# Optimization experiments

Measured on AMD Instinct MI355X. Metric: run time of the kernel, lower is better.

Reference implementation:

```python
import jax, jax.numpy as jnp
import numpy as np

B, N, C = 8, 1024, 768
H = 12
HD = C // H  # 64
SCALE = HD ** -0.5


def setup_inputs() -> dict:
    key = jax.random.key(0)
    k1, k2, k3, k4 = jax.random.split(key, 4)
    x = jax.random.normal(k1, (B, N, C), dtype=jnp.float32)
    # torch Linear weights are [out, in]; qkv has no bias (qkv_bias=False)
    w_qkv = jax.random.normal(k2, (3 * C, C), dtype=jnp.float32) * (C ** -0.5)
    w_proj = jax.random.normal(k3, (C, C), dtype=jnp.float32) * (C ** -0.5)
    b_proj = jax.random.normal(k4, (C,), dtype=jnp.float32) * 0.01
    return {"x": x, "w_qkv": w_qkv, "w_proj": w_proj, "b_proj": b_proj}


def reference(x, w_qkv, w_proj, b_proj):
    b, n, c = x.shape
    # qkv: [B, N, 3C] -> [3, B, H, N, HD]
    qkv = (x @ w_qkv.T).reshape(b, n, 3, H, c // H).transpose(2, 0, 3, 1, 4)
    q, k, v = qkv[0], qkv[1], qkv[2]
    attn = jnp.einsum('bhqd,bhkd->bhqk', q, k) * SCALE
    attn = jax.nn.softmax(attn, axis=-1)
    out = jnp.einsum('bhqk,bhkd->bhqd', attn, v)          # [B, H, N, HD]
    out = out.transpose(0, 2, 1, 3).reshape(b, n, c)      # [B, N, C]
    out = out @ w_proj.T + b_proj
    return out
```

## Files before the change

### kernel.cpp

```cpp
#include <hip/hip_runtime.h>
#include <hip/hip_bf16.h>
#include <cstdint>

#define TB 8
#define TN 1024
#define TC 768
#define TH 12
#define THD 64
#define TM (TB*TN)
#define TNQKV (3*TC)
#define QSCALE_LOG2E 0.18033688011112042f
#define THR_BITS 11.541560327111708f

typedef __attribute__((ext_vector_type(8))) short s16x8;
typedef __attribute__((ext_vector_type(4))) short s16x4;
typedef __attribute__((ext_vector_type(4))) float f32x4;
typedef __attribute__((ext_vector_type(16))) float f32x16;
typedef __attribute__((ext_vector_type(2))) unsigned int u32x2;

__device__ __forceinline__ unsigned short f2bf(float f) {
    union { float f; unsigned int u; } v; v.f = f;
    unsigned int u = v.u;
    return (unsigned short)((u + 0x7FFFu + ((u >> 16) & 1u)) >> 16);
}

__device__ __forceinline__ float bf2f(unsigned short h) {
    union { float f; unsigned int u; } v; v.u = ((unsigned int)h) << 16;
    return v.f;
}

__device__ __forceinline__ unsigned int cvt_pk_bf16(float lo, float hi) {
    unsigned int r;
    asm("v_cvt_pk_bf16_f32 %0, %1, %2" : "=v"(r) : "v"(lo), "v"(hi));
    return r;
}

__device__ __forceinline__ void gload_lds16(const unsigned short* g, unsigned short* l) {
    __builtin_amdgcn_global_load_lds(
        (const __attribute__((address_space(1))) unsigned int*)g,
        (__attribute__((address_space(3))) unsigned int*)l,
        16, 0, 0);
}

__global__ __launch_bounds__(256) void cvt3_kernel(
    const float* __restrict__ a, unsigned short* __restrict__ oa, int na,
    const float* __restrict__ b, unsigned short* __restrict__ ob, int nb,
    const float* __restrict__ c, unsigned short* __restrict__ oc, int nc)
{
    int i = blockIdx.x * blockDim.x + threadIdx.x;
    const float* src; unsigned short* dst; int idx;
    if (i < na)           { src = a; dst = oa; idx = i; }
    else if (i < na + nb) { src = b; dst = ob; idx = i - na; }
    else if (i < na + nb + nc) { src = c; dst = oc; idx = i - na - nb; }
    else return;
    f32x4 x0 = *(const f32x4*)(src + (size_t)idx * 8);
    f32x4 x1 = *(const f32x4*)(src + (size_t)idx * 8 + 4);
    s16x8 r;
    #pragma unroll
    for (int e = 0; e < 4; e++) r[e] = (short)f2bf(x0[e]);
    #pragma unroll
    for (int e = 0; e < 4; e++) r[4 + e] = (short)f2bf(x1[e]);
    *(s16x8*)(dst + (size_t)idx * 8) = r;
}

template<bool BIAS, bool OBF16, bool VSPLIT>
__global__ __launch_bounds__(256) void gemm_bt(
    const unsigned short* __restrict__ A,
    const unsigned short* __restrict__ Bm,
    void* __restrict__ Cout,
    const float* __restrict__ bias,
    unsigned short* __restrict__ vt,
    int M, int Nn, int K)
{
    __shared__ unsigned short As[128 * 64];
    __shared__ unsigned short Bs[128 * 64];
    const int t = threadIdx.x;
    const int w = t >> 6, l = t & 63;
    const int lh = l >> 4;
    const int wm = w >> 1, wn = w & 1;
    const int bm = blockIdx.x, bn = blockIdx.y;
    const int l31 = l & 31, khi = l >> 5;
    const int r7 = l31 & 7;

    f32x16 acc00 = {}, acc01 = {}, acc10 = {}, acc11 = {};

    const unsigned short* Ab = A + (size_t)bm * 128 * K;
    const unsigned short* Bb = Bm + (size_t)bn * 128 * K;

    for (int kt = 0; kt < K; kt += 64) {
        __syncthreads();
        #pragma unroll
        for (int j = 0; j < 4; j++) {
            const int s = j * 256 + t, row = s >> 3, c = s & 7;
            const int g = c ^ (row & 7);
            gload_lds16(Ab + (size_t)row * K + kt + g * 8, As + s * 8);
            gload_lds16(Bb + (size_t)row * K + kt + g * 8, Bs + s * 8);
        }
        __syncthreads();
        #pragma unroll
        for (int ks = 0; ks < 4; ks++) {
            const int ch = ((ks << 1) + khi) ^ r7;
            const unsigned short* Ar = As + (wm * 64 + l31) * 64 + ch * 8;
            const unsigned short* Br = Bs + (wn * 64 + l31) * 64 + ch * 8;
            s16x8 a0 = *(const s16x8*)(Ar);
            s16x8 a1 = *(const s16x8*)(Ar + 32 * 64);
            s16x8 b0 = *(const s16x8*)(Br);
            s16x8 b1 = *(const s16x8*)(Br + 32 * 64);
            acc00 = __builtin_amdgcn_mfma_f32_32x32x16_bf16(a0, b0, acc00, 0, 0, 0);
            acc01 = __builtin_amdgcn_mfma_f32_32x32x16_bf16(a0, b1, acc01, 0, 0, 0);
            acc10 = __builtin_amdgcn_mfma_f32_32x32x16_bf16(a1, b0, acc10, 0, 0, 0);
            acc11 = __builtin_amdgcn_mfma_f32_32x32x16_bf16(a1, b1, acc11, 0, 0, 0);
        }
    }

    const int r0 = bm * 128 + wm * 64;
    const int c0 = bn * 128 + wn * 64;
    f32x16 accs[2][2] = {{acc00, acc01}, {acc10, acc11}};
    if constexpr (VSPLIT) {
        if (bn >= 12) {
            const int bb = (r0 >> 10) * TH;
            #pragma unroll
            for (int X = 0; X < 2; X++)
                #pragma unroll
                for (int Y = 0; Y < 2; Y++) {
                    const int dg = c0 + Y * 32 + l31 - 2 * TC;
                    unsigned short* vp = vt + ((size_t)(bb + (dg >> 6)) << 16)
                                            + (dg & 63) * TN;
                    const int k0 = (r0 & 1023) + X * 32 + 4 * khi;
                    #pragma unroll
                    for (int g = 0; g < 4; g++) {
                        u32x2 r;
                        r[0] = cvt_pk_bf16(accs[X][Y][g * 4], accs[X][Y][g * 4 + 1]);
                        r[1] = cvt_pk_bf16(accs[X][Y][g * 4 + 2], accs[X][Y][g * 4 + 3]);
                        *(u32x2*)(vp + k0 + 8 * g) = r;
                    }
                }
            return;
        }
    }
    if constexpr (OBF16) {
        unsigned short* O = (unsigned short*)Cout;
        #pragma unroll
        for (int X = 0; X < 2; X++)
            #pragma unroll
            for (int Y = 0; Y < 2; Y++) {
                const int cc = c0 + Y * 32 + l31;
                const int rb = r0 + X * 32 + 4 * khi;
                #pragma unroll
                for (int i = 0; i < 16; i++)
                    O[(size_t)(rb + (i & 3) + 8 * (i >> 2)) * Nn + cc] =
                        f2bf(accs[X][Y][i]);
            }
    } else {
        float* O = (float*)Cout;
        #pragma unroll
        for (int X = 0; X < 2; X++)
            #pragma unroll
            for (int Y = 0; Y < 2; Y++) {
                const int cc = c0 + Y * 32 + l31;
                const int rb = r0 + X * 32 + 4 * khi;
                float bv = 0.f;
                if constexpr (BIAS) bv = bias[cc];
                #pragma unroll
                for (int i = 0; i < 16; i++)
                    O[(size_t)(rb + (i & 3) + 8 * (i >> 2)) * Nn + cc] =
                        accs[X][Y][i] + bv;
            }
    }
}

__global__ __launch_bounds__(512) void attn_kernel(
    const unsigned short* __restrict__ qkv,
    const unsigned short* __restrict__ vt,
    unsigned short* __restrict__ out)
{
    const int bid = blockIdx.x;
    const int vid = (bid & 7) * 96 + (bid >> 3);
    const int bh = vid >> 3;
    const int qt = vid & 7;
    const int b = bh / TH, h = bh % TH;
    const int t = threadIdx.x, w = t >> 6, l = t & 63;
    const int lr = l & 15, lh = l >> 4;
    const int qbase = qt * 128 + w * 16;

    __shared__ unsigned short Kbuf[2][64 * 64];
    __shared__ unsigned short Vbuf[2][64 * 64];
    __shared__ unsigned short plds[8][16 * 64];

    const unsigned short* kbase = qkv + (size_t)(b * TN) * TNQKV + TC + h * THD;
    const unsigned short* vtb = vt + (size_t)bh * THD * TN;

    const int srow_lo = (l >> 3);
    const int schunk = (l & 7) ^ srow_lo;
    const int srow = w * 8 + srow_lo;
    const int sdst = w * 512 + l * 8;

    const unsigned short* qptr = qkv + (size_t)(b * TN + qbase + lr) * TNQKV + h * THD;
    s16x8 bq[2];
    #pragma unroll
    for (int cj = 0; cj < 2; cj++) {
        s16x8 raw = *(const s16x8*)(qptr + cj * 32 + lh * 8);
        #pragma unroll
        for (int e = 0; e < 8; e++)
            bq[cj][e] = (short)f2bf(bf2f((unsigned short)raw[e]) * QSCALE_LOG2E);
    }
    s16x8 av1;
    #pragma unroll
    for (int e = 0; e < 8; e++) av1[e] = (short)0x3F80;

    f32x4 o[5] = {};
    float m2 = -1e30f;
    unsigned short* pw = plds[w];
    const int lr7 = lr & 7;

    gload_lds16(kbase + (size_t)srow * TNQKV + schunk * 8, &Kbuf[0][sdst]);
    gload_lds16(vtb + (size_t)srow * TN + schunk * 8, &Vbuf[0][sdst]);
    __syncthreads();

    for (int it = 0; it < 16; it++) {
        const int kt = it * 64;
        const int cur = it & 1, nxt = cur ^ 1;
        {
            const int ktn = (kt + 64) & (TN - 1);
            gload_lds16(kbase + (size_t)(ktn + srow) * TNQKV + schunk * 8, &Kbuf[nxt][sdst]);
            gload_lds16(vtb + (size_t)srow * TN + ktn + schunk * 8, &Vbuf[nxt][sdst]);
        }
        const unsigned short* Kc = Kbuf[cur];
        const unsigned short* Vc = Vbuf[cur];

        f32x4 s[4];
        #pragma unroll
        for (int kk = 0; kk < 4; kk++) {
            const int r = kk * 16 + lr;
            s16x8 ak0 = *(const s16x8*)(Kc + r * 64 + ((lh ^ lr7) * 8));
            s16x8 ak1 = *(const s16x8*)(Kc + r * 64 + (((4 + lh) ^ lr7) * 8));
            f32x4 z = {0.f, 0.f, 0.f, 0.f};
            z = __builtin_amdgcn_mfma_f32_16x16x32_bf16(ak0, bq[0], z, 0, 0, 0);
            z = __builtin_amdgcn_mfma_f32_16x16x32_bf16(ak1, bq[1], z, 0, 0, 0);
            s[kk] = z;
        }

        float v[16];
        #pragma unroll
        for (int kk = 0; kk < 4; kk++)
            #pragma unroll
            for (int i = 0; i < 4; i++) v[kk * 4 + i] = s[kk][i];
        float mx = fmaxf(fmaxf(v[0], v[1]), v[2]);
        #pragma unroll
        for (int j = 3; j + 1 < 16; j += 2) mx = fmaxf(fmaxf(mx, v[j]), v[j + 1]);
        mx = fmaxf(mx, v[15]);
        if (!__all(mx <= m2 + THR_BITS)) {
            float rmx = fmaxf(mx, __shfl_xor(mx, 16, 64));
            rmx = fmaxf(rmx, __shfl_xor(rmx, 32, 64));
            float newm = fmaxf(m2, rmx);
            float corr = __builtin_amdgcn_exp2f(m2 - newm);
            m2 = newm;
            #pragma unroll
            for (int nd = 0; nd < 5; nd++)
                #pragma unroll
                for (int i = 0; i < 4; i++) o[nd][i] *= corr;
        }
        #pragma unroll
        for (int kk = 0; kk < 4; kk++)
            #pragma unroll
            for (int i = 0; i < 4; i++)
                s[kk][i] = __builtin_amdgcn_exp2f(s[kk][i] - m2);

        #pragma unroll
        for (int kk = 0; kk < 4; kk++) {
            u32x2 pk;
            pk[0] = cvt_pk_bf16(s[kk][0], s[kk][1]);
            pk[1] = cvt_pk_bf16(s[kk][2], s[kk][3]);
            const int wch = ((kk << 1) + (lh >> 1)) ^ lr7;
            *(u32x2*)(pw + lr * 64 + wch * 8 + (lh & 1) * 4) = pk;
        }
        #pragma unroll
        for (int ktile = 0; ktile < 2; ktile++) {
            const int rch = ((ktile << 2) + lh) ^ lr7;
            s16x8 bp = *(const s16x8*)(pw + lr * 64 + rch * 8);
            #pragma unroll
            for (int nd = 0; nd < 4; nd++) {
                const int d = nd * 16 + lr;
                s16x8 av = *(const s16x8*)(
                    Vc + d * 64 + ((((ktile << 2) + lh) ^ lr7) * 8));
                o[nd] = __builtin_amdgcn_mfma_f32_16x16x32_bf16(av, bp, o[nd], 0, 0, 0);
            }
            o[4] = __builtin_amdgcn_mfma_f32_16x16x32_bf16(av1, bp, o[4], 0, 0, 0);
        }
        __syncthreads();
    }

    float inv = 1.f / o[4][0];
    unsigned short* op = out + (size_t)(b * TN + qbase + lr) * TC + h * THD;
    #pragma unroll
    for (int nd = 0; nd < 4; nd++) {
        u32x2 r;
        r[0] = cvt_pk_bf16(o[nd][0] * inv, o[nd][1] * inv);
        r[1] = cvt_pk_bf16(o[nd][2] * inv, o[nd][3] * inv);
        *(u32x2*)(op + nd * 16 + lh * 4) = r;
    }
}

extern "C" void kernel_launch(void* const* d_in, const int* in_sizes, int n_in,
                              void* d_out, int out_size, void* d_ws, size_t ws_size,
                              hipStream_t stream) {
    const float* x      = (const float*)d_in[0];
    const float* w_qkv  = (const float*)d_in[1];
    const float* w_proj = (const float*)d_in[2];
    const float* b_proj = (const float*)d_in[3];
    float* out = (float*)d_out;

    unsigned short* xb   = (unsigned short*)d_ws;
    unsigned short* wqb  = xb   + (size_t)TM * TC;
    unsigned short* wpb  = wqb  + (size_t)TNQKV * TC;
    unsigned short* qkvb = wpb  + (size_t)TC * TC;
    unsigned short* vtb  = qkvb + (size_t)TM * TNQKV;
    unsigned short* aob  = vtb  + (size_t)TB * TH * THD * TN;

    const int na = TM * TC / 8, nb = TNQKV * TC / 8, nc = TC * TC / 8;
    cvt3_kernel<<<(na + nb + nc + 255) / 256, 256, 0, stream>>>(
        x, xb, na, w_qkv, wqb, nb, w_proj, wpb, nc);

    gemm_bt<false, true, true><<<dim3(TM / 128, TNQKV / 128), 256, 0, stream>>>(
        xb, wqb, (void*)qkvb, nullptr, vtb, TM, TNQKV, TC);

    attn_kernel<<<768, 512, 0, stream>>>(qkvb, vtb, aob);

    gemm_bt<true, false, false><<<dim3(TM / 128, TC / 128), 256, 0, stream>>>(
        aob, wpb, (void*)out, b_proj, nullptr, TM, TC, TC);
}
```

Measured before the change: 113.4 us.

## Double-buffer GEMM LDS tiles with 8 waves and prioritize MFMA in attention

The GEMM kernel now uses 512 threads (8 waves, each computing a 32x64 sub-tile) and double-buffers the A/B LDS tiles, so global-to-LDS loads for the next K step overlap the MFMAs of the current one. This removes one barrier per iteration. The attention kernel stops prefetching a wrapped-around tile on its last iteration, and wraps its MFMA sections in s_setprio raises to favour matrix-core issue. In exchange the GEMM doubles its LDS use to 64KB per block, which may lower occupancy, and each wave gets less register-level reuse.

```diff
diff --git a/kernel.cpp b/kernel.cpp
--- a/kernel.cpp
+++ b/kernel.cpp
@@ -13,7 +13,6 @@
 #define THR_BITS 11.541560327111708f
 
 typedef __attribute__((ext_vector_type(8))) short s16x8;
-typedef __attribute__((ext_vector_type(4))) short s16x4;
 typedef __attribute__((ext_vector_type(4))) float f32x4;
 typedef __attribute__((ext_vector_type(16))) float f32x16;
 typedef __attribute__((ext_vector_type(2))) unsigned int u32x2;
@@ -64,7 +63,7 @@
 }
 
 template<bool BIAS, bool OBF16, bool VSPLIT>
-__global__ __launch_bounds__(256) void gemm_bt(
+__global__ __launch_bounds__(512) void gemm_bt(
     const unsigned short* __restrict__ A,
     const unsigned short* __restrict__ Bm,
     void* __restrict__ Cout,
@@ -72,100 +71,99 @@
     unsigned short* __restrict__ vt,
     int M, int Nn, int K)
 {
-    __shared__ unsigned short As[128 * 64];
-    __shared__ unsigned short Bs[128 * 64];
+    __shared__ unsigned short As[2][128 * 64];
+    __shared__ unsigned short Bs[2][128 * 64];
     const int t = threadIdx.x;
     const int w = t >> 6, l = t & 63;
-    const int lh = l >> 4;
-    const int wm = w >> 1, wn = w & 1;
+    const int wm = w & 3, wn = w >> 2;
     const int bm = blockIdx.x, bn = blockIdx.y;
     const int l31 = l & 31, khi = l >> 5;
     const int r7 = l31 & 7;
 
-    f32x16 acc00 = {}, acc01 = {}, acc10 = {}, acc11 = {};
+    f32x16 acc0 = {}, acc1 = {};
 
     const unsigned short* Ab = A + (size_t)bm * 128 * K;
     const unsigned short* Bb = Bm + (size_t)bn * 128 * K;
 
-    for (int kt = 0; kt < K; kt += 64) {
-        __syncthreads();
-        #pragma unroll
-        for (int j = 0; j < 4; j++) {
-            const int s = j * 256 + t, row = s >> 3, c = s & 7;
+    auto stage = [&](int bufi, int kt) {
+        #pragma unroll
+        for (int j = 0; j < 2; j++) {
+            const int s = j * 512 + t, row = s >> 3, c = s & 7;
             const int g = c ^ (row & 7);
-            gload_lds16(Ab + (size_t)row * K + kt + g * 8, As + s * 8);
-            gload_lds16(Bb + (size_t)row * K + kt + g * 8, Bs + s * 8);
-        }
-        __syncthreads();
+            gload_lds16(Ab + (size_t)row * K + kt + g * 8, &As[bufi][s * 8]);
+            gload_lds16(Bb + (size_t)row * K + kt + g * 8, &Bs[bufi][s * 8]);
+        }
+    };
+
+    stage(0, 0);
+    __syncthreads();
+
+    const int nkt = K / 64;
+    for (int it = 0; it < nkt; it++) {
+        const int cur = it & 1, nxt = cur ^ 1;
+        if (it + 1 < nkt) stage(nxt, (it + 1) * 64);
+        const unsigned short* Ac = As[cur];
+        const unsigned short* Bc = Bs[cur];
         #pragma unroll
         for (int ks = 0; ks < 4; ks++) {
             const int ch = ((ks << 1) + khi) ^ r7;
-            const unsigned short* Ar = As + (wm * 64 + l31) * 64 + ch * 8;
-            const unsigned short* Br = Bs + (wn * 64 + l31) * 64 + ch * 8;
-            s16x8 a0 = *(const s16x8*)(Ar);
-            s16x8 a1 = *(const s16x8*)(Ar + 32 * 64);
+            s16x8 a0 = *(const s16x8*)(Ac + (wm * 32 + l31) * 64 + ch * 8);
+            const unsigned short* Br = Bc + (wn * 64 + l31) * 64 + ch * 8;
             s16x8 b0 = *(const s16x8*)(Br);
             s16x8 b1 = *(const s16x8*)(Br + 32 * 64);
-            acc00 = __builtin_amdgcn_mfma_f32_32x32x16_bf16(a0, b0, acc00, 0, 0, 0);
-            acc01 = __builtin_amdgcn_mfma_f32_32x32x16_bf16(a0, b1, acc01, 0, 0, 0);
-            acc10 = __builtin_amdgcn_mfma_f32_32x32x16_bf16(a1, b0, acc10, 0, 0, 0);
-            acc11 = __builtin_amdgcn_mfma_f32_32x32x16_bf16(a1, b1, acc11, 0, 0, 0);
-        }
-    }
-
-    const int r0 = bm * 128 + wm * 64;
+            acc0 = __builtin_amdgcn_mfma_f32_32x32x16_bf16(a0, b0, acc0, 0, 0, 0);
+            acc1 = __builtin_amdgcn_mfma_f32_32x32x16_bf16(a0, b1, acc1, 0, 0, 0);
+        }
+        __syncthreads();
+    }
+
+    const int r0 = bm * 128 + wm * 32;
     const int c0 = bn * 128 + wn * 64;
-    f32x16 accs[2][2] = {{acc00, acc01}, {acc10, acc11}};
+    f32x16 accs[2] = {acc0, acc1};
     if constexpr (VSPLIT) {
         if (bn >= 12) {
             const int bb = (r0 >> 10) * TH;
-            #pragma unroll
-            for (int X = 0; X < 2; X++)
+            const int k0 = (r0 & 1023) + 4 * khi;
+            #pragma unroll
+            for (int Y = 0; Y < 2; Y++) {
+                const int dg = c0 + Y * 32 + l31 - 2 * TC;
+                unsigned short* vp = vt + ((size_t)(bb + (dg >> 6)) << 16)
+                                        + (dg & 63) * TN;
                 #pragma unroll
-                for (int Y = 0; Y < 2; Y++) {
-                    const int dg = c0 + Y * 32 + l31 - 2 * TC;
-                    unsigned short* vp = vt + ((size_t)(bb + (dg >> 6)) << 16)
-                                            + (dg & 63) * TN;
-                    const int k0 = (r0 & 1023) + X * 32 + 4 * khi;
-                    #pragma unroll
-                    for (int g = 0; g < 4; g++) {
-                        u32x2 r;
-                        r[0] = cvt_pk_bf16(accs[X][Y][g * 4], accs[X][Y][g * 4 + 1]);
-                        r[1] = cvt_pk_bf16(accs[X][Y][g * 4 + 2], accs[X][Y][g * 4 + 3]);
-                        *(u32x2*)(vp + k0 + 8 * g) = r;
-                    }
+                for (int g = 0; g < 4; g++) {
+                    u32x2 r;
+                    r[0] = cvt_pk_bf16(accs[Y][g * 4], accs[Y][g * 4 + 1]);
+                    r[1] = cvt_pk_bf16(accs[Y][g * 4 + 2], accs[Y][g * 4 + 3]);
+                    *(u32x2*)(vp + k0 + 8 * g) = r;
                 }
+            }
             return;
         }
     }
     if constexpr (OBF16) {
         unsigned short* O = (unsigned short*)Cout;
         #pragma unroll
-        for (int X = 0; X < 2; X++)
-            #pragma unroll
-            for (int Y = 0; Y < 2; Y++) {
-                const int cc = c0 + Y * 32 + l31;
-                const int rb = r0 + X * 32 + 4 * khi;
-                #pragma unroll
-                for (int i = 0; i < 16; i++)
-                    O[(size_t)(rb + (i & 3) + 8 * (i >> 2)) * Nn + cc] =
-                        f2bf(accs[X][Y][i]);
-            }
+        for (int Y = 0; Y < 2; Y++) {
+            const int cc = c0 + Y * 32 + l31;
+            const int rb = r0 + 4 * khi;
+            #pragma unroll
+            for (int i = 0; i < 16; i++)
+                O[(size_t)(rb + (i & 3) + 8 * (i >> 2)) * Nn + cc] =
+                    f2bf(accs[Y][i]);
+        }
     } else {
         float* O = (float*)Cout;
         #pragma unroll
-        for (int X = 0; X < 2; X++)
-            #pragma unroll
-            for (int Y = 0; Y < 2; Y++) {
-                const int cc = c0 + Y * 32 + l31;
-                const int rb = r0 + X * 32 + 4 * khi;
-                float bv = 0.f;
-                if constexpr (BIAS) bv = bias[cc];
-                #pragma unroll
-                for (int i = 0; i < 16; i++)
-                    O[(size_t)(rb + (i & 3) + 8 * (i >> 2)) * Nn + cc] =
-                        accs[X][Y][i] + bv;
-            }
+        for (int Y = 0; Y < 2; Y++) {
+            const int cc = c0 + Y * 32 + l31;
+            const int rb = r0 + 4 * khi;
+            float bv = 0.f;
+            if constexpr (BIAS) bv = bias[cc];
+            #pragma unroll
+            for (int i = 0; i < 16; i++)
+                O[(size_t)(rb + (i & 3) + 8 * (i >> 2)) * Nn + cc] =
+                    accs[Y][i] + bv;
+        }
     }
 }
 
@@ -220,8 +218,8 @@
     for (int it = 0; it < 16; it++) {
         const int kt = it * 64;
         const int cur = it & 1, nxt = cur ^ 1;
-        {
-            const int ktn = (kt + 64) & (TN - 1);
+        if (it + 1 < 16) {
+            const int ktn = kt + 64;
             gload_lds16(kbase + (size_t)(ktn + srow) * TNQKV + schunk * 8, &Kbuf[nxt][sdst]);
             gload_lds16(vtb + (size_t)srow * TN + ktn + schunk * 8, &Vbuf[nxt][sdst]);
         }
@@ -229,6 +227,7 @@
         const unsigned short* Vc = Vbuf[cur];
 
         f32x4 s[4];
+        __builtin_amdgcn_s_setprio(1);
         #pragma unroll
         for (int kk = 0; kk < 4; kk++) {
             const int r = kk * 16 + lr;
@@ -239,6 +238,7 @@
             z = __builtin_amdgcn_mfma_f32_16x16x32_bf16(ak1, bq[1], z, 0, 0, 0);
             s[kk] = z;
         }
+        __builtin_amdgcn_s_setprio(0);
 
         float v[16];
         #pragma unroll
@@ -274,6 +274,7 @@
             const int wch = ((kk << 1) + (lh >> 1)) ^ lr7;
             *(u32x2*)(pw + lr * 64 + wch * 8 + (lh & 1) * 4) = pk;
         }
+        __builtin_amdgcn_s_setprio(1);
         #pragma unroll
         for (int ktile = 0; ktile < 2; ktile++) {
             const int rch = ((ktile << 2) + lh) ^ lr7;
@@ -287,6 +288,7 @@
             }
             o[4] = __builtin_amdgcn_mfma_f32_16x16x32_bf16(av1, bp, o[4], 0, 0, 0);
         }
+        __builtin_amdgcn_s_setprio(0);
         __syncthreads();
     }
 
@@ -321,11 +323,11 @@
     cvt3_kernel<<<(na + nb + nc + 255) / 256, 256, 0, stream>>>(
         x, xb, na, w_qkv, wqb, nb, w_proj, wpb, nc);
 
-    gemm_bt<false, true, true><<<dim3(TM / 128, TNQKV / 128), 256, 0, stream>>>(
+    gemm_bt<false, true, true><<<dim3(TM / 128, TNQKV / 128), 512, 0, stream>>>(
         xb, wqb, (void*)qkvb, nullptr, vtb, TM, TNQKV, TC);
 
     attn_kernel<<<768, 512, 0, stream>>>(qkvb, vtb, aob);
 
-    gemm_bt<true, false, false><<<dim3(TM / 128, TC / 128), 256, 0, stream>>>(
+    gemm_bt<true, false, false><<<dim3(TM / 128, TC / 128), 512, 0, stream>>>(
         aob, wpb, (void*)out, b_proj, nullptr, TM, TC, TC);
 }
```

Measured after the change: 115.1 us. Within noise of the previous version (+1.5%).

## Enlarge GEMM M-tile to 256, add MFMA priority hints and skip wasted prefetch

Applied to the files above, without the earlier changes.

The GEMM kernel now computes a 256x128 tile per block, with each wave holding a 4x2 grid of 32x32 accumulators. This raises data reuse from LDS and halves the grid size for both projections. The cost is more registers and LDS per block, and fewer blocks, which can hurt occupancy and load balance (the proj GEMM drops to 192 blocks). The attention kernel also wraps its MFMA sections in s_setprio hints and skips the useless prefetch on the last iteration.

```diff
diff --git a/kernel.cpp b/kernel.cpp
--- a/kernel.cpp
+++ b/kernel.cpp
@@ -13,7 +13,6 @@
 #define THR_BITS 11.541560327111708f
 
 typedef __attribute__((ext_vector_type(8))) short s16x8;
-typedef __attribute__((ext_vector_type(4))) short s16x4;
 typedef __attribute__((ext_vector_type(4))) float f32x4;
 typedef __attribute__((ext_vector_type(16))) float f32x16;
 typedef __attribute__((ext_vector_type(2))) unsigned int u32x2;
@@ -72,76 +71,84 @@
     unsigned short* __restrict__ vt,
     int M, int Nn, int K)
 {
-    __shared__ unsigned short As[128 * 64];
+    __shared__ unsigned short As[256 * 64];
     __shared__ unsigned short Bs[128 * 64];
     const int t = threadIdx.x;
     const int w = t >> 6, l = t & 63;
-    const int lh = l >> 4;
     const int wm = w >> 1, wn = w & 1;
     const int bm = blockIdx.x, bn = blockIdx.y;
     const int l31 = l & 31, khi = l >> 5;
     const int r7 = l31 & 7;
 
-    f32x16 acc00 = {}, acc01 = {}, acc10 = {}, acc11 = {};
-
-    const unsigned short* Ab = A + (size_t)bm * 128 * K;
+    f32x16 acc[4][2] = {};
+
+    const unsigned short* Ab = A + (size_t)bm * 256 * K;
     const unsigned short* Bb = Bm + (size_t)bn * 128 * K;
 
     for (int kt = 0; kt < K; kt += 64) {
         __syncthreads();
+        #pragma unroll
+        for (int j = 0; j < 8; j++) {
+            const int s = j * 256 + t, row = s >> 3, c = s & 7;
+            const int g = c ^ (row & 7);
+            gload_lds16(Ab + (size_t)row * K + kt + g * 8, As + s * 8);
+        }
         #pragma unroll
         for (int j = 0; j < 4; j++) {
             const int s = j * 256 + t, row = s >> 3, c = s & 7;
             const int g = c ^ (row & 7);
-            gload_lds16(Ab + (size_t)row * K + kt + g * 8, As + s * 8);
             gload_lds16(Bb + (size_t)row * K + kt + g * 8, Bs + s * 8);
         }
         __syncthreads();
         #pragma unroll
         for (int ks = 0; ks < 4; ks++) {
             const int ch = ((ks << 1) + khi) ^ r7;
-            const unsigned short* Ar = As + (wm * 64 + l31) * 64 + ch * 8;
-            const unsigned short* Br = Bs + (wn * 64 + l31) * 64 + ch * 8;
-            s16x8 a0 = *(const s16x8*)(Ar);
-            s16x8 a1 = *(const s16x8*)(Ar + 32 * 64);
-            s16x8 b0 = *(const s16x8*)(Br);
-            s16x8 b1 = *(const s16x8*)(Br + 32 * 64);
-            acc00 = __builtin_amdgcn_mfma_f32_32x32x16_bf16(a0, b0, acc00, 0, 0, 0);
-            acc01 = __builtin_amdgcn_mfma_f32_32x32x16_bf16(a0, b1, acc01, 0, 0, 0);
-            acc10 = __builtin_amdgcn_mfma_f32_32x32x16_bf16(a1, b0, acc10, 0, 0, 0);
-            acc11 = __builtin_amdgcn_mfma_f32_32x32x16_bf16(a1, b1, acc11, 0, 0, 0);
-        }
-    }
-
-    const int r0 = bm * 128 + wm * 64;
+            s16x8 af[4], bf[2];
+            #pragma unroll
+            for (int X = 0; X < 4; X++)
+                af[X] = *(const s16x8*)(As + (wm * 128 + X * 32 + l31) * 64 + ch * 8);
+            #pragma unroll
+            for (int Y = 0; Y < 2; Y++)
+                bf[Y] = *(const s16x8*)(Bs + (wn * 64 + Y * 32 + l31) * 64 + ch * 8);
+            #pragma unroll
+            for (int X = 0; X < 4; X++)
+                #pragma unroll
+                for (int Y = 0; Y < 2; Y++)
+                    acc[X][Y] = __builtin_amdgcn_mfma_f32_32x32x16_bf16(
+                        af[X], bf[Y], acc[X][Y], 0, 0, 0);
+        }
+    }
+
+    const int r0 = bm * 256 + wm * 128;
     const int c0 = bn * 128 + wn * 64;
-    f32x16 accs[2][2] = {{acc00, acc01}, {acc10, acc11}};
     if constexpr (VSPLIT) {
         if (bn >= 12) {
-            const int bb = (r0 >> 10) * TH;
-            #pragma unroll
-            for (int X = 0; X < 2; X++)
+            #pragma unroll
+            for (int X = 0; X < 4; X++) {
+                const int rx = r0 + X * 32;
+                const int bb = (rx >> 10) * TH;
+                const int k0 = (rx & 1023) + 4 * khi;
                 #pragma unroll
                 for (int Y = 0; Y < 2; Y++) {
                     const int dg = c0 + Y * 32 + l31 - 2 * TC;
                     unsigned short* vp = vt + ((size_t)(bb + (dg >> 6)) << 16)
                                             + (dg & 63) * TN;
-                    const int k0 = (r0 & 1023) + X * 32 + 4 * khi;
                     #pragma unroll
                     for (int g = 0; g < 4; g++) {
                         u32x2 r;
-                        r[0] = cvt_pk_bf16(accs[X][Y][g * 4], accs[X][Y][g * 4 + 1]);
-                        r[1] = cvt_pk_bf16(accs[X][Y][g * 4 + 2], accs[X][Y][g * 4 + 3]);
+                        r[0] = cvt_pk_bf16(acc[X][Y][g * 4], acc[X][Y][g * 4 + 1]);
+                        r[1] = cvt_pk_bf16(acc[X][Y][g * 4 + 2], acc[X][Y][g * 4 + 3]);
                         *(u32x2*)(vp + k0 + 8 * g) = r;
                     }
                 }
+            }
             return;
         }
     }
     if constexpr (OBF16) {
         unsigned short* O = (unsigned short*)Cout;
         #pragma unroll
-        for (int X = 0; X < 2; X++)
+        for (int X = 0; X < 4; X++)
             #pragma unroll
             for (int Y = 0; Y < 2; Y++) {
                 const int cc = c0 + Y * 32 + l31;
@@ -149,12 +156,12 @@
                 #pragma unroll
                 for (int i = 0; i < 16; i++)
                     O[(size_t)(rb + (i & 3) + 8 * (i >> 2)) * Nn + cc] =
-                        f2bf(accs[X][Y][i]);
+                        f2bf(acc[X][Y][i]);
             }
     } else {
         float* O = (float*)Cout;
         #pragma unroll
-        for (int X = 0; X < 2; X++)
+        for (int X = 0; X < 4; X++)
             #pragma unroll
             for (int Y = 0; Y < 2; Y++) {
                 const int cc = c0 + Y * 32 + l31;
@@ -164,7 +171,7 @@
                 #pragma unroll
                 for (int i = 0; i < 16; i++)
                     O[(size_t)(rb + (i & 3) + 8 * (i >> 2)) * Nn + cc] =
-                        accs[X][Y][i] + bv;
+                        acc[X][Y][i] + bv;
             }
     }
 }
@@ -220,8 +227,8 @@
     for (int it = 0; it < 16; it++) {
         const int kt = it * 64;
         const int cur = it & 1, nxt = cur ^ 1;
-        {
-            const int ktn = (kt + 64) & (TN - 1);
+        if (it + 1 < 16) {
+            const int ktn = kt + 64;
             gload_lds16(kbase + (size_t)(ktn + srow) * TNQKV + schunk * 8, &Kbuf[nxt][sdst]);
             gload_lds16(vtb + (size_t)srow * TN + ktn + schunk * 8, &Vbuf[nxt][sdst]);
         }
@@ -229,6 +236,7 @@
         const unsigned short* Vc = Vbuf[cur];
 
         f32x4 s[4];
+        __builtin_amdgcn_s_setprio(1);
         #pragma unroll
         for (int kk = 0; kk < 4; kk++) {
             const int r = kk * 16 + lr;
@@ -239,6 +247,7 @@
             z = __builtin_amdgcn_mfma_f32_16x16x32_bf16(ak1, bq[1], z, 0, 0, 0);
             s[kk] = z;
         }
+        __builtin_amdgcn_s_setprio(0);
 
         float v[16];
         #pragma unroll
@@ -274,6 +283,7 @@
             const int wch = ((kk << 1) + (lh >> 1)) ^ lr7;
             *(u32x2*)(pw + lr * 64 + wch * 8 + (lh & 1) * 4) = pk;
         }
+        __builtin_amdgcn_s_setprio(1);
         #pragma unroll
         for (int ktile = 0; ktile < 2; ktile++) {
             const int rch = ((ktile << 2) + lh) ^ lr7;
@@ -287,6 +297,7 @@
             }
             o[4] = __builtin_amdgcn_mfma_f32_16x16x32_bf16(av1, bp, o[4], 0, 0, 0);
         }
+        __builtin_amdgcn_s_setprio(0);
         __syncthreads();
     }
 
@@ -321,11 +332,11 @@
     cvt3_kernel<<<(na + nb + nc + 255) / 256, 256, 0, stream>>>(
         x, xb, na, w_qkv, wqb, nb, w_proj, wpb, nc);
 
-    gemm_bt<false, true, true><<<dim3(TM / 128, TNQKV / 128), 256, 0, stream>>>(
+    gemm_bt<false, true, true><<<dim3(TM / 256, TNQKV / 128), 256, 0, stream>>>(
         xb, wqb, (void*)qkvb, nullptr, vtb, TM, TNQKV, TC);
 
     attn_kernel<<<768, 512, 0, stream>>>(qkvb, vtb, aob);
 
-    gemm_bt<true, false, false><<<dim3(TM / 128, TC / 128), 256, 0, stream>>>(
+    gemm_bt<true, false, false><<<dim3(TM / 256, TC / 128), 256, 0, stream>>>(
         aob, wpb, (void*)out, b_proj, nullptr, TM, TC, TC);
 }
```

Measured after the change: 136.8 us. +20.6%, slower.
